# Performance work log

Hardware: AMD Instinct MI355X
Metric: run time of the kernel (lower is better)

## Reference

```python
import jax, jax.numpy as jnp
import numpy as np

B, S, D, H = 2, 2048, 2048, 16
DH = D // H  # 128
EPS = 1e-6


def _rms_norm(x, w):
    # RMSNorm over last dim with learnable scale
    var = jnp.mean(jnp.square(x), axis=-1, keepdims=True)
    return x * jax.lax.rsqrt(var + EPS) * w


def _apply_rope(x, angles):
    # x: [B, S, H, DH]; angles: [S, DH//2]; interleaved pair rotation
    xs = x.reshape(*x.shape[:-1], DH // 2, 2)
    x0, x1 = xs[..., 0], xs[..., 1]
    cos = jnp.cos(angles)[None, :, None, :]  # [1,S,1,DH/2]
    sin = jnp.sin(angles)[None, :, None, :]
    r0 = x0 * cos - x1 * sin
    r1 = x0 * sin + x1 * cos
    return jnp.stack([r0, r1], axis=-1).reshape(x.shape)


def setup_inputs() -> dict:
    key = jax.random.key(0)
    ks = jax.random.split(key, 4)
    x = jax.random.normal(ks[0], (B, S, D), dtype=jnp.float32)
    # standard RoPE angle table: pos * inv_freq
    inv_freq = 1.0 / (10000.0 ** (jnp.arange(0, DH, 2, dtype=jnp.float32) / DH))
    pos = jnp.arange(S, dtype=jnp.float32)
    rp_freqs = pos[:, None] * inv_freq[None, :]  # [S, DH/2]
    Win = jax.random.normal(ks[1], (3 * D, D), dtype=jnp.float32) * (D ** -0.5)
    b_in = jnp.zeros((3 * D,), dtype=jnp.float32)
    Wout = jax.random.normal(ks[2], (D, D), dtype=jnp.float32) * (D ** -0.5)
    b_out = jnp.zeros((D,), dtype=jnp.float32)
    qk_w = jnp.ones((DH,), dtype=jnp.float32)
    out_w = jnp.ones((D,), dtype=jnp.float32)
    return {"x": x, "rp_freqs": rp_freqs, "Win": Win, "b_in": b_in,
            "Wout": Wout, "b_out": b_out, "qk_w": qk_w, "out_w": out_w}


def reference(x, rp_freqs, Win, b_in, Wout, b_out, qk_w, out_w):
    b, s, d = x.shape
    qkv = jnp.einsum('bsd,ed->bse', x, Win) + b_in  # [B,S,3D]
    qkv = qkv.reshape(b, s, 3, H, DH)
    q, k, v = qkv[:, :, 0], qkv[:, :, 1], qkv[:, :, 2]  # each [B,S,H,DH]
    q = _apply_rope(q, rp_freqs)
    k = _apply_rope(k, rp_freqs)
    q = _rms_norm(q, qk_w)
    k = _rms_norm(k, qk_w)
    # causal SDPA, scale = 1/sqrt(DH) (default)
    a = jax.nn.dot_product_attention(q, k, v, is_causal=True)  # [B,S,H,DH]
    a = a.reshape(b, s, d)
    a = _rms_norm(a, out_w)
    return jnp.einsum('bsd,ed->bse', a, Wout) + b_out
```

## Files before the change

### kernel.cpp

```cpp
#include <hip/hip_runtime.h>
#include <cstdint>
#include <cstddef>

#define Bq  2
#define Sq  2048
#define Dq  2048
#define Hq  16
#define DHq 128
#define E3q 6144

typedef __attribute__((ext_vector_type(8))) short s16x8;
typedef __attribute__((ext_vector_type(4))) float f32x4;

__device__ __forceinline__ unsigned short f2bf(float f){
  union { float f; unsigned u; } v; v.f = f;
  unsigned r = v.u + 0x7FFFu + ((v.u >> 16) & 1u);
  return (unsigned short)(r >> 16);
}
__device__ __forceinline__ float bf2f(unsigned short b){
  union { unsigned u; float f; } v; v.u = ((unsigned)b) << 16;
  return v.f;
}
__device__ __forceinline__ unsigned cvtpk_bf16(float lo, float hi){
  unsigned r;
  asm("v_cvt_pk_bf16_f32 %0, %1, %2" : "=v"(r) : "v"(lo), "v"(hi));
  return r;
}

__device__ __forceinline__ void gload_lds16(const void* g, void* l){
  __builtin_amdgcn_global_load_lds(
      (const __attribute__((address_space(1))) void*)g,
      (__attribute__((address_space(3))) void*)l, 16, 0, 0);
}

__global__ __launch_bounds__(256) void k_convert3(const float* __restrict__ x,
                                                  const float* __restrict__ win,
                                                  const float* __restrict__ wout,
                                                  unsigned short* __restrict__ xb,
                                                  unsigned short* __restrict__ wb,
                                                  unsigned short* __restrict__ woutb){
  const int NX = (Bq*Sq*Dq)/4;
  const int NW = (E3q*Dq)/4;
  const int NO = (Dq*Dq)/4;
  const int total = NX + NW + NO;
  int stride = gridDim.x * blockDim.x;
  for (int i = blockIdx.x*blockDim.x + threadIdx.x; i < total; i += stride){
    const float* src; unsigned short* dst; int j;
    if (i < NX){ src = x; dst = xb; j = i; }
    else if (i < NX+NW){ src = win; dst = wb; j = i - NX; }
    else { src = wout; dst = woutb; j = i - NX - NW; }
    float4 v = reinterpret_cast<const float4*>(src)[j];
    ushort4 o;
    o.x = f2bf(v.x); o.y = f2bf(v.y); o.z = f2bf(v.z); o.w = f2bf(v.w);
    reinterpret_cast<ushort4*>(dst)[j] = o;
  }
}

__global__ __launch_bounds__(512, 1) void k_gemm1_8ph(const unsigned short* __restrict__ A,
                                                      const unsigned short* __restrict__ Bt,
                                                      const float* __restrict__ bias,
                                                      unsigned short* __restrict__ C){
  const int K = 2048, N = 6144;
  const int bid = blockIdx.x;
  const int xcd = bid & 7, u = bid >> 3;
  const int m0 = (xcd*4 + (u & 3)) * 128;
  const int n0 = (u >> 2) * 384;

  const int tid = threadIdx.x;
  const int lane = tid & 63, w = tid >> 6, g = lane >> 4, c = lane & 15;
  const int wm = w >> 2, wn = w & 3;

  __shared__ __align__(16) unsigned short L[65536];

  const int srow = tid >> 2, spc = tid & 3;
  const int ssw = (spc ^ ((srow >> 1) & 3)) << 3;
  const unsigned short* aSrc  = A  + (size_t)(m0 + srow      )*K + ssw;
  const unsigned short* bSrc0 = Bt + (size_t)(n0 + srow      )*K + ssw;
  const unsigned short* bSrc1 = Bt + (size_t)(n0 + srow + 128)*K + ssw;
  const unsigned short* bSrc2 = Bt + (size_t)(n0 + srow + 256)*K + ssw;

  auto stA = [&](int t, int h){
    gload_lds16(aSrc + t*64 + h*32, &L[((t&1)*2 + h)*4096 + tid*8]);
  };
  auto stB = [&](int t, int h, int uu){
    const unsigned short* s = (uu==0) ? bSrc0 : (uu==1) ? bSrc1 : bSrc2;
    gload_lds16(s + t*64 + h*32, &L[16384 + ((t&1)*2 + h)*12288 + uu*4096 + tid*8]);
  };

  int aoff[4], boff[6];
#pragma unroll
  for (int mf=0; mf<4; ++mf){
    int row = wm*64 + mf*16 + c;
    aoff[mf] = row*32 + ((g ^ ((row>>1)&3)) << 3);
  }
#pragma unroll
  for (int nf=0; nf<6; ++nf){
    int row = wn*96 + nf*16 + c;
    boff[nf] = row*32 + ((g ^ ((row>>1)&3)) << 3);
  }

  f32x4 acc[4][6];
#pragma unroll
  for (int i=0;i<4;i++)
#pragma unroll
    for (int j=0;j<6;j++)
#pragma unroll
      for (int r=0;r<4;r++) acc[i][j][r] = 0.f;

  auto RDA = [&](int b, int h, s16x8* af){
    const int ab = (b*2 + h)*4096;
#pragma unroll
    for (int mf=0; mf<4; ++mf) af[mf] = *(const s16x8*)&L[ab + aoff[mf]];
  };
  auto RDB = [&](int b, int h, int nh, s16x8* bf){
    const int bb = 16384 + (b*2 + h)*12288;
#pragma unroll
    for (int j=0; j<3; ++j) bf[j] = *(const s16x8*)&L[bb + boff[nh*3 + j]];
  };
  auto MM = [&](s16x8* af, s16x8* bf, int nh){
    __builtin_amdgcn_s_setprio(1);
#pragma unroll
    for (int mf=0; mf<4; ++mf)
#pragma unroll
      for (int j=0; j<3; ++j)
        acc[mf][nh*3+j] = __builtin_amdgcn_mfma_f32_16x16x32_bf16(af[mf], bf[j], acc[mf][nh*3+j], 0,0,0);
    __builtin_amdgcn_s_setprio(0);
  };
  auto BAR = [&](){
    __builtin_amdgcn_sched_barrier(0);
    __builtin_amdgcn_s_barrier();
    __builtin_amdgcn_sched_barrier(0);
  };

  stA(0,0); stB(0,0,0); stB(0,0,1); stB(0,0,2);
  stA(0,1); stB(0,1,0); stB(0,1,1); stB(0,1,2);
  stA(1,0); stB(1,0,0); stB(1,0,1); stB(1,0,2);
  asm volatile("s_waitcnt vmcnt(4)" ::: "memory");
  __builtin_amdgcn_s_barrier();

  for (int i=0; i<16; ++i){
    const int T0 = 2*i, T1 = 2*i + 1;
    const bool st = (i < 15);
    s16x8 af[4], bf[3];
    RDA(0,0,af); RDB(0,0,0,bf);
    stA(T1,1); stB(T1,1,0);
    BAR(); MM(af,bf,0); BAR();
    RDB(0,0,1,bf);
    stB(T1,1,1); stB(T1,1,2);
    BAR(); MM(af,bf,1); BAR();
    RDA(0,1,af); RDB(0,1,0,bf);
    if (st){ stA(T0+2,0); stB(T0+2,0,0); }
    BAR(); MM(af,bf,0); BAR();
    RDB(0,1,1,bf);
    if (st){ stB(T0+2,0,1); stB(T0+2,0,2); }
    __builtin_amdgcn_sched_barrier(0);
    if (st) asm volatile("s_waitcnt vmcnt(4)" ::: "memory");
    else    asm volatile("s_waitcnt vmcnt(0)" ::: "memory");
    BAR(); MM(af,bf,1); BAR();
    RDA(1,0,af); RDB(1,0,0,bf);
    if (st){ stA(T0+2,1); stB(T0+2,1,0); }
    BAR(); MM(af,bf,0); BAR();
    RDB(1,0,1,bf);
    if (st){ stB(T0+2,1,1); stB(T0+2,1,2); }
    BAR(); MM(af,bf,1); BAR();
    RDA(1,1,af); RDB(1,1,0,bf);
    if (st){ stA(T1+2,0); stB(T1+2,0,0); }
    BAR(); MM(af,bf,0); BAR();
    RDB(1,1,1,bf);
    if (st){ stB(T1+2,0,1); stB(T1+2,0,2); }
    __builtin_amdgcn_sched_barrier(0);
    if (st) asm volatile("s_waitcnt vmcnt(4)" ::: "memory");
    else    asm volatile("s_waitcnt vmcnt(0)" ::: "memory");
    BAR(); MM(af,bf,1); BAR();
  }

#pragma unroll
  for (int nf=0; nf<6; ++nf){
    const int col = n0 + wn*96 + nf*16 + c;
    const float bv = bias[col];
#pragma unroll
    for (int mf=0; mf<4; ++mf){
      const int row = m0 + wm*64 + mf*16 + g*4;
#pragma unroll
      for (int r=0; r<4; ++r)
        C[(size_t)(row+r)*N + col] = f2bf(acc[mf][nf][r] + bv);
    }
  }
}

__global__ __launch_bounds__(512, 1) void k_gemm2_8ph(const unsigned short* __restrict__ A,
                                                      const unsigned short* __restrict__ Bt,
                                                      const float* __restrict__ bias,
                                                      float* __restrict__ C){
  const int K = 2048, N = 2048, NI = 16;
  const int bid = blockIdx.x;
  const int xcd = bid & 7, u = bid >> 3;
  const int m0 = (xcd*4 + (u & 3)) * 128;
  const int n0 = (u >> 2) * 256;

  const int tid = threadIdx.x;
  const int lane = tid & 63, w = tid >> 6, g = lane >> 4, c = lane & 15;
  const int wm = w >> 2, wn = w & 3;

  __shared__ __align__(16) unsigned short L[49152];

  const int srow = tid >> 2, spc = tid & 3;
  const int ssw = (spc ^ ((srow >> 1) & 3)) << 3;
  const unsigned short* aSrc  = A  + (size_t)(m0 + srow      )*K + ssw;
  const unsigned short* bSrc0 = Bt + (size_t)(n0 + srow      )*K + ssw;
  const unsigned short* bSrc1 = Bt + (size_t)(n0 + srow + 128)*K + ssw;

  auto stA = [&](int t, int h){
    gload_lds16(aSrc + t*64 + h*32, &L[((t&1)*2 + h)*4096 + tid*8]);
  };
  auto stB = [&](int t, int h, int uu){
    const unsigned short* s = (uu==0) ? bSrc0 : bSrc1;
    gload_lds16(s + t*64 + h*32, &L[16384 + ((t&1)*2 + h)*8192 + uu*4096 + tid*8]);
  };

  int aoff[4], boff[4];
#pragma unroll
  for (int mf=0; mf<4; ++mf){
    int row = wm*64 + mf*16 + c;
    aoff[mf] = row*32 + ((g ^ ((row>>1)&3)) << 3);
  }
#pragma unroll
  for (int nf=0; nf<4; ++nf){
    int row = wn*64 + nf*16 + c;
    boff[nf] = row*32 + ((g ^ ((row>>1)&3)) << 3);
  }

  f32x4 acc[4][4];
#pragma unroll
  for (int i=0;i<4;i++)
#pragma unroll
    for (int j=0;j<4;j++)
#pragma unroll
      for (int r=0;r<4;r++) acc[i][j][r] = 0.f;

  auto RDA = [&](int b, int h, s16x8* af){
    const int ab = (b*2 + h)*4096;
#pragma unroll
    for (int mf=0; mf<4; ++mf) af[mf] = *(const s16x8*)&L[ab + aoff[mf]];
  };
  auto RDB = [&](int b, int h, int nh, s16x8* bf){
    const int bb = 16384 + (b*2 + h)*8192;
#pragma unroll
    for (int j=0; j<2; ++j) bf[j] = *(const s16x8*)&L[bb + boff[nh*2 + j]];
  };
  auto MM = [&](s16x8* af, s16x8* bf, int nh){
    __builtin_amdgcn_s_setprio(1);
#pragma unroll
    for (int mf=0; mf<4; ++mf)
#pragma unroll
      for (int j=0; j<2; ++j)
        acc[mf][nh*2+j] = __builtin_amdgcn_mfma_f32_16x16x32_bf16(af[mf], bf[j], acc[mf][nh*2+j], 0,0,0);
    __builtin_amdgcn_s_setprio(0);
  };
  auto BAR = [&](){
    __builtin_amdgcn_sched_barrier(0);
    __builtin_amdgcn_s_barrier();
    __builtin_amdgcn_sched_barrier(0);
  };

  stA(0,0); stB(0,0,0); stB(0,0,1);
  stA(0,1); stB(0,1,0); stB(0,1,1);
  stA(1,0); stB(1,0,0); stB(1,0,1);
  asm volatile("s_waitcnt vmcnt(3)" ::: "memory");
  __builtin_amdgcn_s_barrier();

  for (int i=0; i<NI; ++i){
    const int T0 = 2*i, T1 = 2*i + 1;
    const bool st = (i < NI-1);
    s16x8 af[4], bf[2];
    RDA(0,0,af); RDB(0,0,0,bf);
    stA(T1,1); stB(T1,1,0);
    BAR(); MM(af,bf,0); BAR();
    RDB(0,0,1,bf);
    stB(T1,1,1);
    BAR(); MM(af,bf,1); BAR();
    RDA(0,1,af); RDB(0,1,0,bf);
    if (st){ stA(T0+2,0); stB(T0+2,0,0); }
    BAR(); MM(af,bf,0); BAR();
    RDB(0,1,1,bf);
    if (st){ stB(T0+2,0,1); }
    __builtin_amdgcn_sched_barrier(0);
    if (st) asm volatile("s_waitcnt vmcnt(3)" ::: "memory");
    else    asm volatile("s_waitcnt vmcnt(0)" ::: "memory");
    BAR(); MM(af,bf,1); BAR();
    RDA(1,0,af); RDB(1,0,0,bf);
    if (st){ stA(T0+2,1); stB(T0+2,1,0); }
    BAR(); MM(af,bf,0); BAR();
    RDB(1,0,1,bf);
    if (st){ stB(T0+2,1,1); }
    BAR(); MM(af,bf,1); BAR();
    RDA(1,1,af); RDB(1,1,0,bf);
    if (st){ stA(T1+2,0); stB(T1+2,0,0); }
    BAR(); MM(af,bf,0); BAR();
    RDB(1,1,1,bf);
    if (st){ stB(T1+2,0,1); }
    __builtin_amdgcn_sched_barrier(0);
    if (st) asm volatile("s_waitcnt vmcnt(3)" ::: "memory");
    else    asm volatile("s_waitcnt vmcnt(0)" ::: "memory");
    BAR(); MM(af,bf,1); BAR();
  }

#pragma unroll
  for (int nf=0; nf<4; ++nf){
    const int col = n0 + wn*64 + nf*16 + c;
    const float bv = bias[col];
#pragma unroll
    for (int mf=0; mf<4; ++mf){
      const int row = m0 + wm*64 + mf*16 + g*4;
#pragma unroll
      for (int r=0; r<4; ++r)
        C[(size_t)(row+r)*N + col] = acc[mf][nf][r] + bv;
    }
  }
}

__global__ __launch_bounds__(256) void k_rope_qk(const unsigned short* __restrict__ QKV,
                                                 const float* __restrict__ rp,
                                                 const float* __restrict__ qk_w,
                                                 unsigned short* __restrict__ Qp,
                                                 unsigned short* __restrict__ Kp){
  const int p = threadIdx.x;
  const int s = blockIdx.x*4 + threadIdx.y;
  const int h = blockIdx.y;
  const int b = blockIdx.z;
  const size_t n = (size_t)b*Sq + s;
  const int bh = b*Hq + h;

  float ang = rp[s*64 + p];
  float sn, cs; sincosf(ang, &sn, &cs);
  float w0 = qk_w[2*p], w1 = qk_w[2*p+1];
  const float QSCALE = 0.08838834764831845f * 1.4426950408889634f;

  {
    unsigned q01 = *(const unsigned*)&QKV[n*E3q + h*DHq + 2*p];
    float x0 = bf2f((unsigned short)(q01 & 0xFFFFu));
    float x1 = bf2f((unsigned short)(q01 >> 16));
    float r0 = x0*cs - x1*sn, r1 = x0*sn + x1*cs;
    float ss = r0*r0 + r1*r1;
#pragma unroll
    for (int m=1;m<64;m<<=1) ss += __shfl_xor(ss, m);
    float sc = rsqrtf(ss/128.f + 1e-6f) * QSCALE;
    unsigned short o0 = f2bf(r0*sc*w0), o1 = f2bf(r1*sc*w1);
    *(unsigned*)&Qp[((size_t)bh*Sq + s)*DHq + 2*p] = (unsigned)o0 | ((unsigned)o1<<16);
  }
  {
    unsigned k01 = *(const unsigned*)&QKV[n*E3q + Dq + h*DHq + 2*p];
    float x0 = bf2f((unsigned short)(k01 & 0xFFFFu));
    float x1 = bf2f((unsigned short)(k01 >> 16));
    float r0 = x0*cs - x1*sn, r1 = x0*sn + x1*cs;
    float ss = r0*r0 + r1*r1;
#pragma unroll
    for (int m=1;m<64;m<<=1) ss += __shfl_xor(ss, m);
    float sc = rsqrtf(ss/128.f + 1e-6f);
    unsigned short o0 = f2bf(r0*sc*w0), o1 = f2bf(r1*sc*w1);
    *(unsigned*)&Kp[((size_t)bh*Sq + s)*DHq + 2*p] = (unsigned)o0 | ((unsigned)o1<<16);
  }
}

__global__ __launch_bounds__(256) void k_transpose_v(const unsigned short* __restrict__ QKV,
                                                     unsigned short* __restrict__ Vt){
  const int sblk = blockIdx.x;
  const int bh = blockIdx.y;
  const int b = bh >> 4, h = bh & 15;
  const int tid = threadIdx.x;
  __shared__ unsigned short T[128][136];

  const size_t base = ((size_t)(b*Sq) + sblk*128) * E3q + 2*(size_t)Dq + h*DHq;
#pragma unroll
  for (int i=0;i<8;i++){
    int pk = tid + i*256;
    int row = pk >> 4, cc = (pk & 15) * 8;
    s16x8 v = *(const s16x8*)&QKV[base + (size_t)row*E3q + cc];
    *(s16x8*)&T[row][cc] = v;
  }
  __syncthreads();
  const int dh = tid >> 1, sh = (tid & 1) * 64;
  unsigned short buf[64];
#pragma unroll
  for (int s=0;s<64;s++) buf[s] = T[sh + s][dh];
  size_t obase = ((size_t)bh*DHq + dh)*Sq + sblk*128 + sh;
#pragma unroll
  for (int i=0;i<8;i++)
    *(s16x8*)&Vt[obase + i*8] = *(const s16x8*)&buf[i*8];
}

__global__ __launch_bounds__(256, 2) void k_attn(const unsigned short* __restrict__ Qp,
                                                 const unsigned short* __restrict__ Kp,
                                                 const unsigned short* __restrict__ Vt,
                                                 unsigned short* __restrict__ Ar){
  const int L = blockIdx.x;
  int bh, qtile;
  if (L < 256){ bh = L >> 3; qtile = 8 + (L & 7); }
  else { int Ml = L - 256; bh = Ml >> 3; qtile = 7 - (Ml & 7); }
  const int b = bh >> 4, h = bh & 15;
  const int tid = threadIdx.x;
  const int w = tid >> 6, lane = tid & 63, g = lane >> 4, c = lane & 15;
  const int r0w = qtile*128 + w*32;

  const unsigned short* Qh = Qp + (size_t)bh * Sq * DHq;
  const unsigned short* Kh = Kp + (size_t)bh * Sq * DHq;
  const unsigned short* Vh = Vt + (size_t)bh * DHq * Sq;

  __shared__ __align__(16) unsigned short Ks[2][64*128];
  __shared__ __align__(16) unsigned short Vs[2][128*64];
  __shared__ __align__(16) unsigned short Pl[4][32*64];
  unsigned short* Pw = &Pl[w][0];

  s16x8 qf[2][4];
#pragma unroll
  for (int mi=0;mi<2;mi++)
#pragma unroll
    for (int kc=0;kc<4;kc++)
      qf[mi][kc] = *(const s16x8*)&Qh[(size_t)(r0w + mi*16 + c)*DHq + kc*32 + g*8];

  f32x4 acc[2][8];
#pragma unroll
  for (int mi=0;mi<2;mi++)
#pragma unroll
    for (int dt=0;dt<8;dt++)
#pragma unroll
      for (int r=0;r<4;r++) acc[mi][dt][r] = 0.f;
  float m_r[2] = { -INFINITY, -INFINITY };
  float l_p[2] = { 0.f, 0.f };

  const int nsteps = 2*qtile + 2;

  auto stage = [&](int j0s, int bufi){
#pragma unroll
    for (int i=0;i<4;i++){
      int pk = tid + i*256;
      int row = pk>>4, pcc = pk&15;
      gload_lds16(&Kh[(size_t)(j0s+row)*DHq + ((pcc^(row&7))<<3)], &Ks[bufi][pk*8]);
    }
#pragma unroll
    for (int i=0;i<4;i++){
      int pk = tid + i*256;
      int row = pk>>3, pcc = pk&7;
      gload_lds16(&Vh[(size_t)row*Sq + j0s + ((pcc^(row&7))<<3)], &Vs[bufi][pk*8]);
    }
  };

  stage(0, 0);
  __syncthreads();

  for (int t=0; t<nsteps; ++t){
    const int j0 = t*64;
    if (t+1 < nsteps) stage((t+1)*64, (t+1)&1);

    if (j0 <= r0w + 31){
      const unsigned short* Kc = &Ks[t&1][0];
      const unsigned short* Vc = &Vs[t&1][0];

      f32x4 sv[2][4];
#pragma unroll
      for (int mi=0;mi<2;mi++)
#pragma unroll
        for (int js=0;js<4;js++)
#pragma unroll
          for (int r=0;r<4;r++) sv[mi][js][r] = 0.f;

      __builtin_amdgcn_s_setprio(1);
#pragma unroll
      for (int js=0;js<4;js++){
        s16x8 kf[4];
#pragma unroll
        for (int kc=0;kc<4;kc++)
          kf[kc] = *(const s16x8*)&Kc[(js*16 + c)*128 + (((kc*4+g)^(c&7))<<3)];
#pragma unroll
        for (int mi=0;mi<2;mi++)
#pragma unroll
          for (int kc=0;kc<4;kc++)
            sv[mi][js] = __builtin_amdgcn_mfma_f32_16x16x32_bf16(kf[kc], qf[mi][kc], sv[mi][js], 0,0,0);
      }
      __builtin_amdgcn_s_setprio(0);

      if (j0 + 63 > r0w){
#pragma unroll
        for (int mi=0;mi<2;mi++){
          const int q = r0w + mi*16 + c;
#pragma unroll
          for (int js=0;js<4;js++)
#pragma unroll
            for (int r=0;r<4;r++)
              if (j0 + js*16 + g*4 + r > q) sv[mi][js][r] = -INFINITY;
        }
      }

      float pmx[2];
#pragma unroll
      for (int mi=0;mi<2;mi++){
        float mx = fmaxf(fmaxf(sv[mi][0][0],sv[mi][0][1]), fmaxf(sv[mi][0][2],sv[mi][0][3]));
#pragma unroll
        for (int js=1;js<4;js++){
          float a = fmaxf(fmaxf(sv[mi][js][0],sv[mi][js][1]), fmaxf(sv[mi][js][2],sv[mi][js][3]));
          mx = fmaxf(mx, a);
        }
        mx = fmaxf(mx, __shfl_xor(mx, 16));
        mx = fmaxf(mx, __shfl_xor(mx, 32));
        pmx[mi] = mx;
      }
      int need = (pmx[0] > m_r[0] + 8.f) | (pmx[1] > m_r[1] + 8.f);
      if (__any(need)){
#pragma unroll
        for (int mi=0;mi<2;mi++){
          float mnew = fmaxf(m_r[mi], pmx[mi]);
          float corr = exp2f(m_r[mi] - mnew);
          l_p[mi] *= corr;
          m_r[mi] = mnew;
#pragma unroll
          for (int dt=0;dt<8;dt++)
#pragma unroll
            for (int r=0;r<4;r++) acc[mi][dt][r] *= corr;
        }
      }
#pragma unroll
      for (int mi=0;mi<2;mi++){
        const float mm = m_r[mi];
        const int rowoff = (mi*16 + c)*64;
#pragma unroll
        for (int js=0;js<4;js++){
          float e0 = exp2f(sv[mi][js][0] - mm);
          float e1 = exp2f(sv[mi][js][1] - mm);
          float e2 = exp2f(sv[mi][js][2] - mm);
          float e3 = exp2f(sv[mi][js][3] - mm);
          l_p[mi] += (e0+e1)+(e2+e3);
          uint2 pk2;
          pk2.x = cvtpk_bf16(e0, e1);
          pk2.y = cvtpk_bf16(e2, e3);
          const int kc8 = js*2 + (g>>1);
          *(uint2*)&Pw[rowoff + ((kc8 ^ (c&7))<<3) + (g&1)*4] = pk2;
        }
      }

      s16x8 pfr[2][2];
#pragma unroll
      for (int mi=0;mi<2;mi++)
#pragma unroll
        for (int kc=0;kc<2;kc++)
          pfr[mi][kc] = *(const s16x8*)&Pw[(mi*16 + c)*64 + (((kc*4+g)^(c&7))<<3)];
      __builtin_amdgcn_s_setprio(1);
#pragma unroll
      for (int dt=0; dt<8; dt++){
#pragma unroll
        for (int kc=0;kc<2;kc++){
          s16x8 vfr = *(const s16x8*)&Vc[(dt*16 + c)*64 + (((kc*4+g)^(c&7))<<3)];
#pragma unroll
          for (int mi=0;mi<2;mi++)
            acc[mi][dt] = __builtin_amdgcn_mfma_f32_16x16x32_bf16(vfr, pfr[mi][kc], acc[mi][dt], 0,0,0);
        }
      }
      __builtin_amdgcn_s_setprio(0);
    }
    __syncthreads();
  }

#pragma unroll
  for (int mi=0;mi<2;mi++){
    float l = l_p[mi];
    l += __shfl_xor(l, 16);
    l += __shfl_xor(l, 32);
    const float inv = 1.f / l;
    const int row = r0w + mi*16 + c;
    unsigned short* dst = &Ar[((size_t)(b*Sq + row))*Dq + h*DHq];
#pragma unroll
    for (int dt=0; dt<8; dt++){
      uint2 o2;
      o2.x = cvtpk_bf16(acc[mi][dt][0]*inv, acc[mi][dt][1]*inv);
      o2.y = cvtpk_bf16(acc[mi][dt][2]*inv, acc[mi][dt][3]*inv);
      *(uint2*)&dst[dt*16 + g*4] = o2;
    }
  }
}

__global__ __launch_bounds__(256) void k_rmsnorm(unsigned short* __restrict__ A,
                                                 const float* __restrict__ w){
  const int row = blockIdx.x;
  const int tid = threadIdx.x;
  s16x8 v = *(const s16x8*)&A[(size_t)row*Dq + tid*8];
  float f[8]; float ss = 0.f;
#pragma unroll
  for (int i=0;i<8;i++){ f[i] = bf2f((unsigned short)v[i]); ss += f[i]*f[i]; }
#pragma unroll
  for (int m=1;m<64;m<<=1) ss += __shfl_xor(ss, m);
  __shared__ float red[4];
  if ((tid&63)==0) red[tid>>6] = ss;
  __syncthreads();
  ss = red[0]+red[1]+red[2]+red[3];
  float sc = rsqrtf(ss/2048.f + 1e-6f);
  unsigned short o[8];
#pragma unroll
  for (int i=0;i<8;i++) o[i] = f2bf(f[i]*sc*w[tid*8+i]);
  *(s16x8*)&A[(size_t)row*Dq + tid*8] = *(const s16x8*)o;
}

extern "C" void kernel_launch(void* const* d_in, const int* in_sizes, int n_in,
                              void* d_out, int out_size, void* d_ws, size_t ws_size,
                              hipStream_t stream){
  const float* x     = (const float*)d_in[0];
  const float* rp    = (const float*)d_in[1];
  const float* Win   = (const float*)d_in[2];
  const float* b_in  = (const float*)d_in[3];
  const float* Wout  = (const float*)d_in[4];
  const float* b_out = (const float*)d_in[5];
  const float* qk_w  = (const float*)d_in[6];
  const float* out_w = (const float*)d_in[7];
  float* outp = (float*)d_out;

  if (ws_size < (160ull<<20)) return;

  char* ws = (char*)d_ws;
  unsigned short* Xb    = (unsigned short*)(ws);
  unsigned short* Wb    = (unsigned short*)(ws + (16ull<<20));
  unsigned short* Woutb = (unsigned short*)(ws + (40ull<<20));
  unsigned short* QKVb  = (unsigned short*)(ws + (48ull<<20));
  unsigned short* Qp    = (unsigned short*)(ws + (96ull<<20));
  unsigned short* Kp    = (unsigned short*)(ws + (112ull<<20));
  unsigned short* Vt    = (unsigned short*)(ws + (128ull<<20));
  unsigned short* Ar    = (unsigned short*)(ws + (144ull<<20));

  k_convert3<<<2048, 256, 0, stream>>>(x, Win, Wout, Xb, Wb, Woutb);
  k_gemm1_8ph<<<512, 512, 0, stream>>>(Xb, Wb, b_in, QKVb);
  k_rope_qk<<<dim3(Sq/4, Hq, Bq), dim3(64,4), 0, stream>>>(QKVb, rp, qk_w, Qp, Kp);
  k_transpose_v<<<dim3(Sq/128, Bq*Hq), 256, 0, stream>>>(QKVb, Vt);
  k_attn<<<512, 256, 0, stream>>>(Qp, Kp, Vt, Ar);
  k_rmsnorm<<<Bq*Sq, 256, 0, stream>>>(Ar, out_w);
  k_gemm2_8ph<<<256, 512, 0, stream>>>(Ar, Woutb, b_out, outp);
}
```

Before: 278.0 us.

## Fuse RoPE, QK-norm and V transpose into QKV GEMM epilogue; fold output RMSNorm

```diff
diff --git a/kernel.cpp b/kernel.cpp
--- a/kernel.cpp
+++ b/kernel.cpp
@@ -36,6 +36,7 @@
 __global__ __launch_bounds__(256) void k_convert3(const float* __restrict__ x,
                                                   const float* __restrict__ win,
                                                   const float* __restrict__ wout,
+                                                  const float* __restrict__ out_w,
                                                   unsigned short* __restrict__ xb,
                                                   unsigned short* __restrict__ wb,
                                                   unsigned short* __restrict__ woutb){
@@ -45,65 +46,76 @@
   const int total = NX + NW + NO;
   int stride = gridDim.x * blockDim.x;
   for (int i = blockIdx.x*blockDim.x + threadIdx.x; i < total; i += stride){
-    const float* src; unsigned short* dst; int j;
-    if (i < NX){ src = x; dst = xb; j = i; }
-    else if (i < NX+NW){ src = win; dst = wb; j = i - NX; }
-    else { src = wout; dst = woutb; j = i - NX - NW; }
-    float4 v = reinterpret_cast<const float4*>(src)[j];
-    ushort4 o;
-    o.x = f2bf(v.x); o.y = f2bf(v.y); o.z = f2bf(v.z); o.w = f2bf(v.w);
-    reinterpret_cast<ushort4*>(dst)[j] = o;
-  }
-}
-
-__global__ __launch_bounds__(512, 1) void k_gemm1_8ph(const unsigned short* __restrict__ A,
-                                                      const unsigned short* __restrict__ Bt,
-                                                      const float* __restrict__ bias,
-                                                      unsigned short* __restrict__ C){
-  const int K = 2048, N = 6144;
+    if (i < NX + NW){
+      const float* src; unsigned short* dst; int j;
+      if (i < NX){ src = x; dst = xb; j = i; }
+      else { src = win; dst = wb; j = i - NX; }
+      float4 v = reinterpret_cast<const float4*>(src)[j];
+      ushort4 o;
+      o.x = f2bf(v.x); o.y = f2bf(v.y); o.z = f2bf(v.z); o.w = f2bf(v.w);
+      reinterpret_cast<ushort4*>(dst)[j] = o;
+    } else {
+      int j = i - NX - NW;
+      float4 v = reinterpret_cast<const float4*>(wout)[j];
+      float4 w = reinterpret_cast<const float4*>(out_w)[j & 511];
+      ushort4 o;
+      o.x = f2bf(v.x*w.x); o.y = f2bf(v.y*w.y); o.z = f2bf(v.z*w.z); o.w = f2bf(v.w*w.w);
+      reinterpret_cast<ushort4*>(woutb)[j] = o;
+    }
+  }
+}
+
+__global__ __launch_bounds__(512, 1) void k_gemm1f(const unsigned short* __restrict__ A,
+                                                   const unsigned short* __restrict__ Bt,
+                                                   const float* __restrict__ bias,
+                                                   const float* __restrict__ rp,
+                                                   const float* __restrict__ qk_w,
+                                                   unsigned short* __restrict__ Qp,
+                                                   unsigned short* __restrict__ Kp,
+                                                   unsigned short* __restrict__ Vt){
+  const int K = 2048, NI = 16;
   const int bid = blockIdx.x;
   const int xcd = bid & 7, u = bid >> 3;
   const int m0 = (xcd*4 + (u & 3)) * 128;
-  const int n0 = (u >> 2) * 384;
+  const int n0 = (u >> 2) * 256;
 
   const int tid = threadIdx.x;
   const int lane = tid & 63, w = tid >> 6, g = lane >> 4, c = lane & 15;
   const int wm = w >> 2, wn = w & 3;
 
-  __shared__ __align__(16) unsigned short L[65536];
+  __shared__ __align__(16) unsigned short L[49152];
 
   const int srow = tid >> 2, spc = tid & 3;
   const int ssw = (spc ^ ((srow >> 1) & 3)) << 3;
   const unsigned short* aSrc  = A  + (size_t)(m0 + srow      )*K + ssw;
   const unsigned short* bSrc0 = Bt + (size_t)(n0 + srow      )*K + ssw;
   const unsigned short* bSrc1 = Bt + (size_t)(n0 + srow + 128)*K + ssw;
-  const unsigned short* bSrc2 = Bt + (size_t)(n0 + srow + 256)*K + ssw;
 
   auto stA = [&](int t, int h){
     gload_lds16(aSrc + t*64 + h*32, &L[((t&1)*2 + h)*4096 + tid*8]);
   };
   auto stB = [&](int t, int h, int uu){
-    const unsigned short* s = (uu==0) ? bSrc0 : (uu==1) ? bSrc1 : bSrc2;
-    gload_lds16(s + t*64 + h*32, &L[16384 + ((t&1)*2 + h)*12288 + uu*4096 + tid*8]);
-  };
-
-  int aoff[4], boff[6];
+    const unsigned short* s = (uu==0) ? bSrc0 : bSrc1;
+    gload_lds16(s + t*64 + h*32, &L[16384 + ((t&1)*2 + h)*8192 + uu*4096 + tid*8]);
+  };
+
+  int aoff[4], boff[4];
 #pragma unroll
   for (int mf=0; mf<4; ++mf){
     int row = wm*64 + mf*16 + c;
     aoff[mf] = row*32 + ((g ^ ((row>>1)&3)) << 3);
   }
 #pragma unroll
-  for (int nf=0; nf<6; ++nf){
-    int row = wn*96 + nf*16 + c;
+  for (int nf=0; nf<4; ++nf){
+    int row = wn*64 + nf*16 + c;
     boff[nf] = row*32 + ((g ^ ((row>>1)&3)) << 3);
   }
 
-  f32x4 acc[4][6];
+  f32x4 acc[4][4];
 #pragma unroll
   for (int i=0;i<4;i++)
 #pragma unroll
-    for (int j=0;j<6;j++)
+    for (int j=0;j<4;j++)
 #pragma unroll
       for (int r=0;r<4;r++) acc[i][j][r] = 0.f;
 
@@ -113,17 +125,17 @@
     for (int mf=0; mf<4; ++mf) af[mf] = *(const s16x8*)&L[ab + aoff[mf]];
   };
   auto RDB = [&](int b, int h, int nh, s16x8* bf){
-    const int bb = 16384 + (b*2 + h)*12288;
-#pragma unroll
-    for (int j=0; j<3; ++j) bf[j] = *(const s16x8*)&L[bb + boff[nh*3 + j]];
+    const int bb = 16384 + (b*2 + h)*8192;
+#pragma unroll
+    for (int j=0; j<2; ++j) bf[j] = *(const s16x8*)&L[bb + boff[nh*2 + j]];
   };
   auto MM = [&](s16x8* af, s16x8* bf, int nh){
     __builtin_amdgcn_s_setprio(1);
 #pragma unroll
     for (int mf=0; mf<4; ++mf)
 #pragma unroll
-      for (int j=0; j<3; ++j)
-        acc[mf][nh*3+j] = __builtin_amdgcn_mfma_f32_16x16x32_bf16(af[mf], bf[j], acc[mf][nh*3+j], 0,0,0);
+      for (int j=0; j<2; ++j)
+        acc[mf][nh*2+j] = __builtin_amdgcn_mfma_f32_16x16x32_bf16(af[mf], bf[j], acc[mf][nh*2+j], 0,0,0);
     __builtin_amdgcn_s_setprio(0);
   };
   auto BAR = [&](){
@@ -132,58 +144,163 @@
     __builtin_amdgcn_sched_barrier(0);
   };
 
-  stA(0,0); stB(0,0,0); stB(0,0,1); stB(0,0,2);
-  stA(0,1); stB(0,1,0); stB(0,1,1); stB(0,1,2);
-  stA(1,0); stB(1,0,0); stB(1,0,1); stB(1,0,2);
-  asm volatile("s_waitcnt vmcnt(4)" ::: "memory");
+  stA(0,0); stB(0,0,0); stB(0,0,1);
+  stA(0,1); stB(0,1,0); stB(0,1,1);
+  stA(1,0); stB(1,0,0); stB(1,0,1);
+  asm volatile("s_waitcnt vmcnt(3)" ::: "memory");
   __builtin_amdgcn_s_barrier();
 
-  for (int i=0; i<16; ++i){
+  for (int i=0; i<NI; ++i){
     const int T0 = 2*i, T1 = 2*i + 1;
-    const bool st = (i < 15);
-    s16x8 af[4], bf[3];
+    const bool st = (i < NI-1);
+    s16x8 af[4], bf[2];
     RDA(0,0,af); RDB(0,0,0,bf);
     stA(T1,1); stB(T1,1,0);
     BAR(); MM(af,bf,0); BAR();
     RDB(0,0,1,bf);
-    stB(T1,1,1); stB(T1,1,2);
+    stB(T1,1,1);
     BAR(); MM(af,bf,1); BAR();
     RDA(0,1,af); RDB(0,1,0,bf);
     if (st){ stA(T0+2,0); stB(T0+2,0,0); }
     BAR(); MM(af,bf,0); BAR();
     RDB(0,1,1,bf);
-    if (st){ stB(T0+2,0,1); stB(T0+2,0,2); }
-    __builtin_amdgcn_sched_barrier(0);
-    if (st) asm volatile("s_waitcnt vmcnt(4)" ::: "memory");
+    if (st){ stB(T0+2,0,1); }
+    __builtin_amdgcn_sched_barrier(0);
+    if (st) asm volatile("s_waitcnt vmcnt(3)" ::: "memory");
     else    asm volatile("s_waitcnt vmcnt(0)" ::: "memory");
     BAR(); MM(af,bf,1); BAR();
     RDA(1,0,af); RDB(1,0,0,bf);
     if (st){ stA(T0+2,1); stB(T0+2,1,0); }
     BAR(); MM(af,bf,0); BAR();
     RDB(1,0,1,bf);
-    if (st){ stB(T0+2,1,1); stB(T0+2,1,2); }
+    if (st){ stB(T0+2,1,1); }
     BAR(); MM(af,bf,1); BAR();
     RDA(1,1,af); RDB(1,1,0,bf);
     if (st){ stA(T1+2,0); stB(T1+2,0,0); }
     BAR(); MM(af,bf,0); BAR();
     RDB(1,1,1,bf);
-    if (st){ stB(T1+2,0,1); stB(T1+2,0,2); }
-    __builtin_amdgcn_sched_barrier(0);
-    if (st) asm volatile("s_waitcnt vmcnt(4)" ::: "memory");
+    if (st){ stB(T1+2,0,1); }
+    __builtin_amdgcn_sched_barrier(0);
+    if (st) asm volatile("s_waitcnt vmcnt(3)" ::: "memory");
     else    asm volatile("s_waitcnt vmcnt(0)" ::: "memory");
     BAR(); MM(af,bf,1); BAR();
   }
 
-#pragma unroll
-  for (int nf=0; nf<6; ++nf){
-    const int col = n0 + wn*96 + nf*16 + c;
-    const float bv = bias[col];
-#pragma unroll
-    for (int mf=0; mf<4; ++mf){
-      const int row = m0 + wm*64 + mf*16 + g*4;
-#pragma unroll
-      for (int r=0; r<4; ++r)
-        C[(size_t)(row+r)*N + col] = f2bf(acc[mf][nf][r] + bv);
+  const int btype = (n0 < 2048) ? 0 : (n0 < 4096) ? 1 : 2;
+  const int b  = m0 >> 11;
+  const int sb = m0 & 2047;
+  const int h0 = (n0 & 2047) >> 7;
+  const int LTS = 264;
+  const float QSCALE = 0.08838834764831845f * 1.4426950408889634f;
+
+#pragma unroll
+  for (int nf=0; nf<4; ++nf){
+    const float bv = bias[n0 + wn*64 + nf*16 + c];
+#pragma unroll
+    for (int mf=0; mf<4; ++mf)
+#pragma unroll
+      for (int r=0; r<4; ++r) acc[mf][nf][r] += bv;
+  }
+
+  __syncthreads();
+
+  if (btype < 2){
+    float s2[4][4];
+#pragma unroll
+    for (int mf=0;mf<4;mf++)
+#pragma unroll
+      for (int r=0;r<4;r++){
+        float s = 0.f;
+#pragma unroll
+        for (int nf=0;nf<4;nf++){ float v = acc[mf][nf][r]; s += v*v; }
+        s2[mf][r] = s;
+      }
+#pragma unroll
+    for (int m=1;m<16;m<<=1)
+#pragma unroll
+      for (int mf=0;mf<4;mf++)
+#pragma unroll
+        for (int r=0;r<4;r++) s2[mf][r] += __shfl_xor(s2[mf][r], m);
+    float* Ssum = (float*)&L[0];
+    if (c==0 && (wn&1)==0){
+#pragma unroll
+      for (int mf=0;mf<4;mf++)
+#pragma unroll
+        for (int r=0;r<4;r++)
+          Ssum[(wm*64+mf*16+g*4+r)*2 + (wn>>1)] = s2[mf][r];
+    }
+    __syncthreads();
+    if (c==0 && (wn&1)==1){
+#pragma unroll
+      for (int mf=0;mf<4;mf++)
+#pragma unroll
+        for (int r=0;r<4;r++)
+          Ssum[(wm*64+mf*16+g*4+r)*2 + (wn>>1)] += s2[mf][r];
+    }
+    __syncthreads();
+    float rsc[4][4];
+#pragma unroll
+    for (int mf=0;mf<4;mf++)
+#pragma unroll
+      for (int r=0;r<4;r++)
+        rsc[mf][r] = rsqrtf(Ssum[(wm*64+mf*16+g*4+r)*2 + (wn>>1)]*(1.f/128.f) + 1e-6f);
+    __syncthreads();
+
+    const float qmul = (btype==0) ? QSCALE : 1.f;
+    float wq[4];
+#pragma unroll
+    for (int nf=0;nf<4;nf++) wq[nf] = qk_w[(wn*64+nf*16+c)&127];
+
+#pragma unroll
+    for (int mf=0;mf<4;mf++)
+#pragma unroll
+      for (int r=0;r<4;r++){
+        const int rowl = wm*64+mf*16+g*4+r;
+        const int s = sb + rowl;
+        const float sc = rsc[mf][r] * qmul;
+#pragma unroll
+        for (int nf=0;nf<4;nf++){
+          const int p = ((wn*64+nf*16+c)&127) >> 1;
+          float sn, cs; __sincosf(rp[s*64+p], &sn, &cs);
+          float v  = acc[mf][nf][r];
+          float pv = __shfl_xor(v, 1);
+          float rot = ((c&1)==0) ? (v*cs - pv*sn) : (pv*sn + v*cs);
+          L[rowl*LTS + wn*64+nf*16+c] = f2bf(rot * sc * wq[nf]);
+        }
+      }
+    __syncthreads();
+    {
+      const int rw = tid >> 2, hd = (tid>>1)&1, hf = tid&1;
+      const int bh = b*Hq + h0 + hd;
+      unsigned short* dst = ((btype==0) ? Qp : Kp)
+                          + ((size_t)bh*Sq + sb + rw)*DHq + hf*64;
+      const unsigned short* srcl = &L[rw*LTS + hd*128 + hf*64];
+#pragma unroll
+      for (int i2=0;i2<8;i2++)
+        *(s16x8*)&dst[i2*8] = *(const s16x8*)&srcl[i2*8];
+    }
+  } else {
+#pragma unroll
+    for (int mf=0;mf<4;mf++)
+#pragma unroll
+      for (int r=0;r<4;r++){
+        const int rowl = wm*64+mf*16+g*4+r;
+#pragma unroll
+        for (int nf=0;nf<4;nf++)
+          L[rowl*LTS + wn*64+nf*16+c] = f2bf(acc[mf][nf][r]);
+      }
+    __syncthreads();
+    {
+      const int dh2 = tid >> 1, hfr = (tid & 1) * 64;
+      const int hd = dh2 >> 7, dh = dh2 & 127;
+      const int bh = b*Hq + h0 + hd;
+      unsigned short buf[64];
+#pragma unroll
+      for (int i2=0;i2<64;i2++) buf[i2] = L[(hfr+i2)*LTS + dh2];
+      unsigned short* dst = Vt + ((size_t)bh*DHq + dh)*Sq + sb + hfr;
+#pragma unroll
+      for (int i2=0;i2<8;i2++)
+        *(s16x8*)&dst[i2*8] = *(const s16x8*)&buf[i2*8];
     }
   }
 }
@@ -191,6 +308,7 @@
 __global__ __launch_bounds__(512, 1) void k_gemm2_8ph(const unsigned short* __restrict__ A,
                                                       const unsigned short* __restrict__ Bt,
                                                       const float* __restrict__ bias,
+                                                      const float* __restrict__ rscale,
                                                       float* __restrict__ C){
   const int K = 2048, N = 2048, NI = 16;
   const int bid = blockIdx.x;
@@ -314,79 +432,28 @@
       const int row = m0 + wm*64 + mf*16 + g*4;
 #pragma unroll
       for (int r=0; r<4; ++r)
-        C[(size_t)(row+r)*N + col] = acc[mf][nf][r] + bv;
-    }
-  }
-}
-
-__global__ __launch_bounds__(256) void k_rope_qk(const unsigned short* __restrict__ QKV,
-                                                 const float* __restrict__ rp,
-                                                 const float* __restrict__ qk_w,
-                                                 unsigned short* __restrict__ Qp,
-                                                 unsigned short* __restrict__ Kp){
-  const int p = threadIdx.x;
-  const int s = blockIdx.x*4 + threadIdx.y;
-  const int h = blockIdx.y;
-  const int b = blockIdx.z;
-  const size_t n = (size_t)b*Sq + s;
-  const int bh = b*Hq + h;
-
-  float ang = rp[s*64 + p];
-  float sn, cs; sincosf(ang, &sn, &cs);
-  float w0 = qk_w[2*p], w1 = qk_w[2*p+1];
-  const float QSCALE = 0.08838834764831845f * 1.4426950408889634f;
-
-  {
-    unsigned q01 = *(const unsigned*)&QKV[n*E3q + h*DHq + 2*p];
-    float x0 = bf2f((unsigned short)(q01 & 0xFFFFu));
-    float x1 = bf2f((unsigned short)(q01 >> 16));
-    float r0 = x0*cs - x1*sn, r1 = x0*sn + x1*cs;
-    float ss = r0*r0 + r1*r1;
-#pragma unroll
-    for (int m=1;m<64;m<<=1) ss += __shfl_xor(ss, m);
-    float sc = rsqrtf(ss/128.f + 1e-6f) * QSCALE;
-    unsigned short o0 = f2bf(r0*sc*w0), o1 = f2bf(r1*sc*w1);
-    *(unsigned*)&Qp[((size_t)bh*Sq + s)*DHq + 2*p] = (unsigned)o0 | ((unsigned)o1<<16);
-  }
-  {
-    unsigned k01 = *(const unsigned*)&QKV[n*E3q + Dq + h*DHq + 2*p];
-    float x0 = bf2f((unsigned short)(k01 & 0xFFFFu));
-    float x1 = bf2f((unsigned short)(k01 >> 16));
-    float r0 = x0*cs - x1*sn, r1 = x0*sn + x1*cs;
-    float ss = r0*r0 + r1*r1;
-#pragma unroll
-    for (int m=1;m<64;m<<=1) ss += __shfl_xor(ss, m);
-    float sc = rsqrtf(ss/128.f + 1e-6f);
-    unsigned short o0 = f2bf(r0*sc*w0), o1 = f2bf(r1*sc*w1);
-    *(unsigned*)&Kp[((size_t)bh*Sq + s)*DHq + 2*p] = (unsigned)o0 | ((unsigned)o1<<16);
-  }
-}
-
-__global__ __launch_bounds__(256) void k_transpose_v(const unsigned short* __restrict__ QKV,
-                                                     unsigned short* __restrict__ Vt){
-  const int sblk = blockIdx.x;
-  const int bh = blockIdx.y;
-  const int b = bh >> 4, h = bh & 15;
+        C[(size_t)(row+r)*N + col] = acc[mf][nf][r]*rscale[row+r] + bv;
+    }
+  }
+}
+
+__global__ __launch_bounds__(256) void k_rowscale(const unsigned short* __restrict__ A,
+                                                  float* __restrict__ sc){
+  const int row = blockIdx.x;
   const int tid = threadIdx.x;
-  __shared__ unsigned short T[128][136];
-
-  const size_t base = ((size_t)(b*Sq) + sblk*128) * E3q + 2*(size_t)Dq + h*DHq;
-#pragma unroll
-  for (int i=0;i<8;i++){
-    int pk = tid + i*256;
-    int row = pk >> 4, cc = (pk & 15) * 8;
-    s16x8 v = *(const s16x8*)&QKV[base + (size_t)row*E3q + cc];
-    *(s16x8*)&T[row][cc] = v;
-  }
+  s16x8 v = *(const s16x8*)&A[(size_t)row*Dq + tid*8];
+  float ss = 0.f;
+#pragma unroll
+  for (int i=0;i<8;i++){ float f = bf2f((unsigned short)v[i]); ss += f*f; }
+#pragma unroll
+  for (int m=1;m<64;m<<=1) ss += __shfl_xor(ss, m);
+  __shared__ float red[4];
+  if ((tid&63)==0) red[tid>>6] = ss;
   __syncthreads();
-  const int dh = tid >> 1, sh = (tid & 1) * 64;
-  unsigned short buf[64];
-#pragma unroll
-  for (int s=0;s<64;s++) buf[s] = T[sh + s][dh];
-  size_t obase = ((size_t)bh*DHq + dh)*Sq + sblk*128 + sh;
-#pragma unroll
-  for (int i=0;i<8;i++)
-    *(s16x8*)&Vt[obase + i*8] = *(const s16x8*)&buf[i*8];
+  if (tid==0){
+    float t = red[0]+red[1]+red[2]+red[3];
+    sc[row] = rsqrtf(t*(1.f/2048.f) + 1e-6f);
+  }
 }
 
 __global__ __launch_bounds__(256, 2) void k_attn(const unsigned short* __restrict__ Qp,
@@ -577,27 +644,6 @@
   }
 }
 
-__global__ __launch_bounds__(256) void k_rmsnorm(unsigned short* __restrict__ A,
-                                                 const float* __restrict__ w){
-  const int row = blockIdx.x;
-  const int tid = threadIdx.x;
-  s16x8 v = *(const s16x8*)&A[(size_t)row*Dq + tid*8];
-  float f[8]; float ss = 0.f;
-#pragma unroll
-  for (int i=0;i<8;i++){ f[i] = bf2f((unsigned short)v[i]); ss += f[i]*f[i]; }
-#pragma unroll
-  for (int m=1;m<64;m<<=1) ss += __shfl_xor(ss, m);
-  __shared__ float red[4];
-  if ((tid&63)==0) red[tid>>6] = ss;
-  __syncthreads();
-  ss = red[0]+red[1]+red[2]+red[3];
-  float sc = rsqrtf(ss/2048.f + 1e-6f);
-  unsigned short o[8];
-#pragma unroll
-  for (int i=0;i<8;i++) o[i] = f2bf(f[i]*sc*w[tid*8+i]);
-  *(s16x8*)&A[(size_t)row*Dq + tid*8] = *(const s16x8*)o;
-}
-
 extern "C" void kernel_launch(void* const* d_in, const int* in_sizes, int n_in,
                               void* d_out, int out_size, void* d_ws, size_t ws_size,
                               hipStream_t stream){
@@ -617,17 +663,15 @@
   unsigned short* Xb    = (unsigned short*)(ws);
   unsigned short* Wb    = (unsigned short*)(ws + (16ull<<20));
   unsigned short* Woutb = (unsigned short*)(ws + (40ull<<20));
-  unsigned short* QKVb  = (unsigned short*)(ws + (48ull<<20));
+  float*          rsc   = (float*)         (ws + (48ull<<20));
   unsigned short* Qp    = (unsigned short*)(ws + (96ull<<20));
   unsigned short* Kp    = (unsigned short*)(ws + (112ull<<20));
   unsigned short* Vt    = (unsigned short*)(ws + (128ull<<20));
   unsigned short* Ar    = (unsigned short*)(ws + (144ull<<20));
 
-  k_convert3<<<2048, 256, 0, stream>>>(x, Win, Wout, Xb, Wb, Woutb);
-  k_gemm1_8ph<<<512, 512, 0, stream>>>(Xb, Wb, b_in, QKVb);
-  k_rope_qk<<<dim3(Sq/4, Hq, Bq), dim3(64,4), 0, stream>>>(QKVb, rp, qk_w, Qp, Kp);
-  k_transpose_v<<<dim3(Sq/128, Bq*Hq), 256, 0, stream>>>(QKVb, Vt);
+  k_convert3<<<2048, 256, 0, stream>>>(x, Win, Wout, out_w, Xb, Wb, Woutb);
+  k_gemm1f<<<768, 512, 0, stream>>>(Xb, Wb, b_in, rp, qk_w, Qp, Kp, Vt);
   k_attn<<<512, 256, 0, stream>>>(Qp, Kp, Vt, Ar);
-  k_rmsnorm<<<Bq*Sq, 256, 0, stream>>>(Ar, out_w);
-  k_gemm2_8ph<<<256, 512, 0, stream>>>(Ar, Woutb, b_out, outp);
-}
+  k_rowscale<<<Bq*Sq, 256, 0, stream>>>(Ar, rsc);
+  k_gemm2_8ph<<<256, 512, 0, stream>>>(Ar, Woutb, b_out, rsc, outp);
+}
```

Result: faster. 269.7 us (-3.0%).

## Fuse RoPE, QK RMSNorm and V transpose into QKV GEMM epilogue; fold output norm

Applied to the files above, without the earlier changes.

```diff
diff --git a/kernel.cpp b/kernel.cpp
--- a/kernel.cpp
+++ b/kernel.cpp
@@ -36,31 +36,57 @@
 __global__ __launch_bounds__(256) void k_convert3(const float* __restrict__ x,
                                                   const float* __restrict__ win,
                                                   const float* __restrict__ wout,
+                                                  const float* __restrict__ out_w,
+                                                  const float* __restrict__ rp,
                                                   unsigned short* __restrict__ xb,
                                                   unsigned short* __restrict__ wb,
-                                                  unsigned short* __restrict__ woutb){
+                                                  unsigned short* __restrict__ woutb,
+                                                  float2* __restrict__ rpcs){
   const int NX = (Bq*Sq*Dq)/4;
   const int NW = (E3q*Dq)/4;
   const int NO = (Dq*Dq)/4;
-  const int total = NX + NW + NO;
+  const int NR = (Sq*64)/4;
+  const int total = NX + NW + NO + NR;
   int stride = gridDim.x * blockDim.x;
   for (int i = blockIdx.x*blockDim.x + threadIdx.x; i < total; i += stride){
-    const float* src; unsigned short* dst; int j;
-    if (i < NX){ src = x; dst = xb; j = i; }
-    else if (i < NX+NW){ src = win; dst = wb; j = i - NX; }
-    else { src = wout; dst = woutb; j = i - NX - NW; }
-    float4 v = reinterpret_cast<const float4*>(src)[j];
-    ushort4 o;
-    o.x = f2bf(v.x); o.y = f2bf(v.y); o.z = f2bf(v.z); o.w = f2bf(v.w);
-    reinterpret_cast<ushort4*>(dst)[j] = o;
-  }
-}
-
-__global__ __launch_bounds__(512, 1) void k_gemm1_8ph(const unsigned short* __restrict__ A,
-                                                      const unsigned short* __restrict__ Bt,
-                                                      const float* __restrict__ bias,
-                                                      unsigned short* __restrict__ C){
-  const int K = 2048, N = 6144;
+    if (i < NX + NW){
+      const float* src; unsigned short* dst; int j;
+      if (i < NX){ src = x; dst = xb; j = i; }
+      else { src = win; dst = wb; j = i - NX; }
+      float4 v = reinterpret_cast<const float4*>(src)[j];
+      ushort4 o;
+      o.x = f2bf(v.x); o.y = f2bf(v.y); o.z = f2bf(v.z); o.w = f2bf(v.w);
+      reinterpret_cast<ushort4*>(dst)[j] = o;
+    } else if (i < NX + NW + NO){
+      int j = i - NX - NW;
+      float4 v = reinterpret_cast<const float4*>(wout)[j];
+      float4 w = reinterpret_cast<const float4*>(out_w)[j & 511];
+      ushort4 o;
+      o.x = f2bf(v.x*w.x); o.y = f2bf(v.y*w.y); o.z = f2bf(v.z*w.z); o.w = f2bf(v.w*w.w);
+      reinterpret_cast<ushort4*>(woutb)[j] = o;
+    } else {
+      int j = i - NX - NW - NO;
+      float4 a = reinterpret_cast<const float4*>(rp)[j];
+      float sn0,cs0,sn1,cs1,sn2,cs2,sn3,cs3;
+      sincosf(a.x,&sn0,&cs0); sincosf(a.y,&sn1,&cs1);
+      sincosf(a.z,&sn2,&cs2); sincosf(a.w,&sn3,&cs3);
+      float4 p0 = make_float4(cs0,sn0,cs1,sn1);
+      float4 p1 = make_float4(cs2,sn2,cs3,sn3);
+      reinterpret_cast<float4*>(rpcs)[j*2  ] = p0;
+      reinterpret_cast<float4*>(rpcs)[j*2+1] = p1;
+    }
+  }
+}
+
+__global__ __launch_bounds__(512, 1) void k_gemm1f(const unsigned short* __restrict__ A,
+                                                   const unsigned short* __restrict__ Bt,
+                                                   const float* __restrict__ bias,
+                                                   const float2* __restrict__ rpcs,
+                                                   const float* __restrict__ qk_w,
+                                                   unsigned short* __restrict__ Qp,
+                                                   unsigned short* __restrict__ Kp,
+                                                   unsigned short* __restrict__ Vt){
+  const int K = 2048;
   const int bid = blockIdx.x;
   const int xcd = bid & 7, u = bid >> 3;
   const int m0 = (xcd*4 + (u & 3)) * 128;
@@ -174,16 +200,80 @@
     BAR(); MM(af,bf,1); BAR();
   }
 
+  const int b  = m0 >> 11;
+  const int sb = m0 & 2047;
+  const int LTS = 390;
+  const float QSCALE = 0.08838834764831845f * 1.4426950408889634f;
+
 #pragma unroll
   for (int nf=0; nf<6; ++nf){
-    const int col = n0 + wn*96 + nf*16 + c;
-    const float bv = bias[col];
-#pragma unroll
-    for (int mf=0; mf<4; ++mf){
-      const int row = m0 + wm*64 + mf*16 + g*4;
-#pragma unroll
-      for (int r=0; r<4; ++r)
-        C[(size_t)(row+r)*N + col] = f2bf(acc[mf][nf][r] + bv);
+    const float bv = bias[n0 + wn*96 + nf*16 + c];
+#pragma unroll
+    for (int mf=0; mf<4; ++mf)
+#pragma unroll
+      for (int r=0; r<4; ++r) acc[mf][nf][r] += bv;
+  }
+
+  __syncthreads();
+
+#pragma unroll
+  for (int mf=0;mf<4;mf++)
+#pragma unroll
+    for (int r=0;r<4;r++){
+      const int rowl = wm*64 + mf*16 + g*4 + r;
+#pragma unroll
+      for (int nf=0;nf<6;nf++)
+        L[rowl*LTS + wn*96 + nf*16 + c] = f2bf(acc[mf][nf][r]);
+    }
+  __syncthreads();
+
+#pragma unroll
+  for (int hd=0; hd<3; ++hd){
+    const int abscol = n0 + hd*128;
+    if (abscol < 4096){
+      const bool isQ = (abscol < 2048);
+      const int bh = b*Hq + ((abscol & 2047) >> 7);
+      const int row = tid >> 2, part = tid & 3;
+      s16x8 vv[4];
+      float ss = 0.f;
+#pragma unroll
+      for (int j=0;j<4;j++){
+        vv[j] = *(const s16x8*)&L[row*LTS + hd*128 + part*32 + j*8];
+#pragma unroll
+        for (int e=0;e<8;e++){ float f = bf2f((unsigned short)vv[j][e]); ss += f*f; }
+      }
+      ss += __shfl_xor(ss, 1);
+      ss += __shfl_xor(ss, 2);
+      const float sc = rsqrtf(ss*(1.f/128.f) + 1e-6f) * (isQ ? QSCALE : 1.f);
+      unsigned short* dst = (isQ ? Qp : Kp) + ((size_t)bh*Sq + sb + row)*DHq + part*32;
+      const float2* rt = rpcs + (size_t)(sb + row)*64;
+#pragma unroll
+      for (int j=0;j<4;j++){
+        unsigned o0,o1,o2,o3;
+#pragma unroll
+        for (int e=0;e<4;e++){
+          const int colh = part*32 + j*8 + 2*e;
+          float v0 = bf2f((unsigned short)vv[j][2*e]);
+          float v1 = bf2f((unsigned short)vv[j][2*e+1]);
+          float2 t = rt[colh>>1];
+          float r0 = (v0*t.x - v1*t.y) * sc * qk_w[colh];
+          float r1 = (v0*t.y + v1*t.x) * sc * qk_w[colh+1];
+          unsigned pk = cvtpk_bf16(r0, r1);
+          if (e==0) o0=pk; else if (e==1) o1=pk; else if (e==2) o2=pk; else o3=pk;
+        }
+        uint4 ov = make_uint4(o0,o1,o2,o3);
+        *(uint4*)&dst[j*8] = ov;
+      }
+    } else {
+      const int bh = b*Hq + ((abscol - 4096) >> 7);
+      const int dh = tid & 127, sh4 = tid >> 7;
+      unsigned short buf[32];
+#pragma unroll
+      for (int i2=0;i2<32;i2++) buf[i2] = L[(sh4*32 + i2)*LTS + hd*128 + dh];
+      unsigned short* dst = Vt + ((size_t)bh*DHq + dh)*Sq + sb + sh4*32;
+#pragma unroll
+      for (int i2=0;i2<4;i2++)
+        *(s16x8*)&dst[i2*8] = *(const s16x8*)&buf[i2*8];
     }
   }
 }
@@ -191,6 +281,7 @@
 __global__ __launch_bounds__(512, 1) void k_gemm2_8ph(const unsigned short* __restrict__ A,
                                                       const unsigned short* __restrict__ Bt,
                                                       const float* __restrict__ bias,
+                                                      const float* __restrict__ rscale,
                                                       float* __restrict__ C){
   const int K = 2048, N = 2048, NI = 16;
   const int bid = blockIdx.x;
@@ -314,79 +405,28 @@
       const int row = m0 + wm*64 + mf*16 + g*4;
 #pragma unroll
       for (int r=0; r<4; ++r)
-        C[(size_t)(row+r)*N + col] = acc[mf][nf][r] + bv;
-    }
-  }
-}
-
-__global__ __launch_bounds__(256) void k_rope_qk(const unsigned short* __restrict__ QKV,
-                                                 const float* __restrict__ rp,
-                                                 const float* __restrict__ qk_w,
-                                                 unsigned short* __restrict__ Qp,
-                                                 unsigned short* __restrict__ Kp){
-  const int p = threadIdx.x;
-  const int s = blockIdx.x*4 + threadIdx.y;
-  const int h = blockIdx.y;
-  const int b = blockIdx.z;
-  const size_t n = (size_t)b*Sq + s;
-  const int bh = b*Hq + h;
-
-  float ang = rp[s*64 + p];
-  float sn, cs; sincosf(ang, &sn, &cs);
-  float w0 = qk_w[2*p], w1 = qk_w[2*p+1];
-  const float QSCALE = 0.08838834764831845f * 1.4426950408889634f;
-
-  {
-    unsigned q01 = *(const unsigned*)&QKV[n*E3q + h*DHq + 2*p];
-    float x0 = bf2f((unsigned short)(q01 & 0xFFFFu));
-    float x1 = bf2f((unsigned short)(q01 >> 16));
-    float r0 = x0*cs - x1*sn, r1 = x0*sn + x1*cs;
-    float ss = r0*r0 + r1*r1;
-#pragma unroll
-    for (int m=1;m<64;m<<=1) ss += __shfl_xor(ss, m);
-    float sc = rsqrtf(ss/128.f + 1e-6f) * QSCALE;
-    unsigned short o0 = f2bf(r0*sc*w0), o1 = f2bf(r1*sc*w1);
-    *(unsigned*)&Qp[((size_t)bh*Sq + s)*DHq + 2*p] = (unsigned)o0 | ((unsigned)o1<<16);
-  }
-  {
-    unsigned k01 = *(const unsigned*)&QKV[n*E3q + Dq + h*DHq + 2*p];
-    float x0 = bf2f((unsigned short)(k01 & 0xFFFFu));
-    float x1 = bf2f((unsigned short)(k01 >> 16));
-    float r0 = x0*cs - x1*sn, r1 = x0*sn + x1*cs;
-    float ss = r0*r0 + r1*r1;
-#pragma unroll
-    for (int m=1;m<64;m<<=1) ss += __shfl_xor(ss, m);
-    float sc = rsqrtf(ss/128.f + 1e-6f);
-    unsigned short o0 = f2bf(r0*sc*w0), o1 = f2bf(r1*sc*w1);
-    *(unsigned*)&Kp[((size_t)bh*Sq + s)*DHq + 2*p] = (unsigned)o0 | ((unsigned)o1<<16);
-  }
-}
-
-__global__ __launch_bounds__(256) void k_transpose_v(const unsigned short* __restrict__ QKV,
-                                                     unsigned short* __restrict__ Vt){
-  const int sblk = blockIdx.x;
-  const int bh = blockIdx.y;
-  const int b = bh >> 4, h = bh & 15;
+        C[(size_t)(row+r)*N + col] = acc[mf][nf][r]*rscale[row+r] + bv;
+    }
+  }
+}
+
+__global__ __launch_bounds__(256) void k_rowscale(const unsigned short* __restrict__ A,
+                                                  float* __restrict__ sc){
+  const int row = blockIdx.x;
   const int tid = threadIdx.x;
-  __shared__ unsigned short T[128][136];
-
-  const size_t base = ((size_t)(b*Sq) + sblk*128) * E3q + 2*(size_t)Dq + h*DHq;
-#pragma unroll
-  for (int i=0;i<8;i++){
-    int pk = tid + i*256;
-    int row = pk >> 4, cc = (pk & 15) * 8;
-    s16x8 v = *(const s16x8*)&QKV[base + (size_t)row*E3q + cc];
-    *(s16x8*)&T[row][cc] = v;
-  }
+  s16x8 v = *(const s16x8*)&A[(size_t)row*Dq + tid*8];
+  float ss = 0.f;
+#pragma unroll
+  for (int i=0;i<8;i++){ float f = bf2f((unsigned short)v[i]); ss += f*f; }
+#pragma unroll
+  for (int m=1;m<64;m<<=1) ss += __shfl_xor(ss, m);
+  __shared__ float red[4];
+  if ((tid&63)==0) red[tid>>6] = ss;
   __syncthreads();
-  const int dh = tid >> 1, sh = (tid & 1) * 64;
-  unsigned short buf[64];
-#pragma unroll
-  for (int s=0;s<64;s++) buf[s] = T[sh + s][dh];
-  size_t obase = ((size_t)bh*DHq + dh)*Sq + sblk*128 + sh;
-#pragma unroll
-  for (int i=0;i<8;i++)
-    *(s16x8*)&Vt[obase + i*8] = *(const s16x8*)&buf[i*8];
+  if (tid==0){
+    float t = red[0]+red[1]+red[2]+red[3];
+    sc[row] = rsqrtf(t*(1.f/2048.f) + 1e-6f);
+  }
 }
 
 __global__ __launch_bounds__(256, 2) void k_attn(const unsigned short* __restrict__ Qp,
@@ -577,27 +617,6 @@
   }
 }
 
-__global__ __launch_bounds__(256) void k_rmsnorm(unsigned short* __restrict__ A,
-                                                 const float* __restrict__ w){
-  const int row = blockIdx.x;
-  const int tid = threadIdx.x;
-  s16x8 v = *(const s16x8*)&A[(size_t)row*Dq + tid*8];
-  float f[8]; float ss = 0.f;
-#pragma unroll
-  for (int i=0;i<8;i++){ f[i] = bf2f((unsigned short)v[i]); ss += f[i]*f[i]; }
-#pragma unroll
-  for (int m=1;m<64;m<<=1) ss += __shfl_xor(ss, m);
-  __shared__ float red[4];
-  if ((tid&63)==0) red[tid>>6] = ss;
-  __syncthreads();
-  ss = red[0]+red[1]+red[2]+red[3];
-  float sc = rsqrtf(ss/2048.f + 1e-6f);
-  unsigned short o[8];
-#pragma unroll
-  for (int i=0;i<8;i++) o[i] = f2bf(f[i]*sc*w[tid*8+i]);
-  *(s16x8*)&A[(size_t)row*Dq + tid*8] = *(const s16x8*)o;
-}
-
 extern "C" void kernel_launch(void* const* d_in, const int* in_sizes, int n_in,
                               void* d_out, int out_size, void* d_ws, size_t ws_size,
                               hipStream_t stream){
@@ -617,17 +636,16 @@
   unsigned short* Xb    = (unsigned short*)(ws);
   unsigned short* Wb    = (unsigned short*)(ws + (16ull<<20));
   unsigned short* Woutb = (unsigned short*)(ws + (40ull<<20));
-  unsigned short* QKVb  = (unsigned short*)(ws + (48ull<<20));
+  float*          rsc   = (float*)         (ws + (48ull<<20));
+  float2*         rpcs  = (float2*)        (ws + (49ull<<20));
   unsigned short* Qp    = (unsigned short*)(ws + (96ull<<20));
   unsigned short* Kp    = (unsigned short*)(ws + (112ull<<20));
   unsigned short* Vt    = (unsigned short*)(ws + (128ull<<20));
   unsigned short* Ar    = (unsigned short*)(ws + (144ull<<20));
 
-  k_convert3<<<2048, 256, 0, stream>>>(x, Win, Wout, Xb, Wb, Woutb);
-  k_gemm1_8ph<<<512, 512, 0, stream>>>(Xb, Wb, b_in, QKVb);
-  k_rope_qk<<<dim3(Sq/4, Hq, Bq), dim3(64,4), 0, stream>>>(QKVb, rp, qk_w, Qp, Kp);
-  k_transpose_v<<<dim3(Sq/128, Bq*Hq), 256, 0, stream>>>(QKVb, Vt);
+  k_convert3<<<2048, 256, 0, stream>>>(x, Win, Wout, out_w, rp, Xb, Wb, Woutb, rpcs);
+  k_gemm1f<<<512, 512, 0, stream>>>(Xb, Wb, b_in, rpcs, qk_w, Qp, Kp, Vt);
   k_attn<<<512, 256, 0, stream>>>(Qp, Kp, Vt, Ar);
-  k_rmsnorm<<<Bq*Sq, 256, 0, stream>>>(Ar, out_w);
-  k_gemm2_8ph<<<256, 512, 0, stream>>>(Ar, Woutb, b_out, outp);
-}
+  k_rowscale<<<Bq*Sq, 256, 0, stream>>>(Ar, rsc);
+  k_gemm2_8ph<<<256, 512, 0, stream>>>(Ar, Woutb, b_out, rsc, outp);
+}
```

After: 278.3 us. Within noise of the previous version (+0.1%).
